# Kernel tuning notes

Measured on AMD Instinct MI355X. Metric: run time of the kernel, lower is better.

## Reference

```python
import jax, jax.numpy as jnp
import numpy as np

B, C, H, W = 4, 256, 64, 64
C8 = C // 8


def setup_inputs() -> dict:
    key = jax.random.key(0)
    k1, k2, k3, k4 = jax.random.split(key, 4)
    x = jax.random.normal(k1, (B, C, H, W), dtype=jnp.float32)
    # conv1d(ks=1, bias=False) projections -> plain [out, in] matrices
    Wq = jax.random.normal(k2, (C8, C), dtype=jnp.float32) * (1.0 / np.sqrt(C))
    Wk = jax.random.normal(k3, (C8, C), dtype=jnp.float32) * (1.0 / np.sqrt(C))
    Wv = jax.random.normal(k4, (C, C), dtype=jnp.float32) * (1.0 / np.sqrt(C))
    gamma = jnp.zeros((1,), dtype=jnp.float32)
    return {"x": x, "Wq": Wq, "Wk": Wk, "Wv": Wv, "gamma": gamma}


def reference(x, Wq, Wk, Wv, gamma):
    b, c, h, w = x.shape
    xf = x.reshape(b, c, h * w)                      # [B, C, N]
    f = jnp.einsum('oc,bcn->bon', Wq, xf)            # [B, C/8, N] query
    g = jnp.einsum('oc,bcn->bon', Wk, xf)            # [B, C/8, N] key
    hv = jnp.einsum('oc,bcn->bon', Wv, xf)           # [B, C,   N] value
    # scores[b,i,j] = sum_c f[b,c,i] * g[b,c,j]; softmax over dim=1 (i)
    scores = jnp.einsum('bci,bcj->bij', f, g)        # [B, N, N]
    beta = jax.nn.softmax(scores, axis=1)
    # o[b,c,j] = sum_i hv[b,c,i] * beta[b,i,j]
    o = jnp.einsum('bci,bij->bcj', hv, beta)         # [B, C, N]
    out = gamma[0] * o + xf
    return out.reshape(b, c, h, w)
```

## Files before the change

### kernel.cpp

```cpp
#include <hip/hip_runtime.h>

#define B_  4
#define C_  256
#define C8_ 32
#define N_  4096

#define TJ 128
#define KI 64
#define SPLITS 4

typedef __attribute__((ext_vector_type(8)))  short bf16x8;
typedef __attribute__((ext_vector_type(16))) float f32x16;

union FragAB { bf16x8 v; unsigned short u[8]; };

__device__ __forceinline__ unsigned short f2bf(float x) {
    unsigned u = __float_as_uint(x);
    unsigned r = u + 0x7FFFu + ((u >> 16) & 1u);
    return (unsigned short)(r >> 16);
}
__device__ __forceinline__ unsigned pack2bf(float a, float b) {
    return (unsigned)f2bf(a) | ((unsigned)f2bf(b) << 16);
}

__global__ __launch_bounds__(256) void prep_w_kernel(
    const float* __restrict__ Wq, const float* __restrict__ Wk,
    const float* __restrict__ Wv, unsigned short* __restrict__ Wbf)
{
    int idx = (blockIdx.x * 256 + threadIdx.x) * 4;
    int row = idx >> 8;
    int col = idx & 255;
    const float* src; int r;
    if (row < 32)      { src = Wq; r = row;      }
    else if (row < 64) { src = Wk; r = row - 32; }
    else               { src = Wv; r = row - 64; }
    float4 v = *(const float4*)&src[r * 256 + col];
    uint2 o; o.x = pack2bf(v.x, v.y); o.y = pack2bf(v.z, v.w);
    *(uint2*)&Wbf[idx] = o;
}

__global__ __launch_bounds__(256) void prep_x_kernel(
    const float* __restrict__ x, unsigned short* __restrict__ xT)
{
    __shared__ unsigned short T[64][66];
    int t  = threadIdx.x;
    int b  = blockIdx.z;
    int c0 = blockIdx.y * 64;
    int n0 = blockIdx.x * 64;
    const float* xb = x + (size_t)b * C_ * N_;
    int n_l = t & 63, c_l = t >> 6;
#pragma unroll
    for (int q = 0; q < 16; ++q) {
        int c = c_l * 16 + q;
        T[n_l][c] = f2bf(xb[(size_t)(c0 + c) * N_ + n0 + n_l]);
    }
    __syncthreads();
    unsigned short* xTb = xT + (size_t)b * N_ * C_;
    int c_l2 = t & 63, nb = t >> 6;
#pragma unroll
    for (int q = 0; q < 16; ++q) {
        int n = nb * 16 + q;
        xTb[(size_t)(n0 + n) * C_ + c0 + c_l2] = T[n][c_l2];
    }
}

__global__ __launch_bounds__(256) void proj_mfma_kernel(
    const unsigned short* __restrict__ Wbf, const unsigned short* __restrict__ xT,
    unsigned short* __restrict__ f, unsigned short* __restrict__ g,
    unsigned short* __restrict__ hv)
{
    int t = threadIdx.x, w = t >> 6, lane = t & 63;
    int half = lane >> 5, l31 = lane & 31;
    int b  = blockIdx.y;
    int n0 = blockIdx.x * 32;

    const unsigned short* xb = xT + ((size_t)b * N_ + n0 + l31) * C_;
    int nm = (w < 2) ? 3 : 2;
    int mt0 = w, mt1 = w + 4, mt2 = w + 8;

    f32x16 acc[3];
#pragma unroll
    for (int a = 0; a < 3; ++a) acc[a] = (f32x16)0.f;

#pragma unroll
    for (int ks = 0; ks < 16; ++ks) {
        int kofs = ks * 16 + half * 8;
        bf16x8 bfr = *(const bf16x8*)&xb[kofs];
        bf16x8 a0 = *(const bf16x8*)&Wbf[(size_t)(mt0 * 32 + l31) * 256 + kofs];
        acc[0] = __builtin_amdgcn_mfma_f32_32x32x16_bf16(a0, bfr, acc[0], 0, 0, 0);
        bf16x8 a1 = *(const bf16x8*)&Wbf[(size_t)(mt1 * 32 + l31) * 256 + kofs];
        acc[1] = __builtin_amdgcn_mfma_f32_32x32x16_bf16(a1, bfr, acc[1], 0, 0, 0);
        if (nm == 3) {
            bf16x8 a2 = *(const bf16x8*)&Wbf[(size_t)(mt2 * 32 + l31) * 256 + kofs];
            acc[2] = __builtin_amdgcn_mfma_f32_32x32x16_bf16(a2, bfr, acc[2], 0, 0, 0);
        }
    }

    unsigned short* fb = f  + (size_t)b * C8_ * N_;
    unsigned short* gb = g  + (size_t)b * C8_ * N_;
    unsigned short* hb = hv + (size_t)b * C_  * N_;
#pragma unroll
    for (int im = 0; im < 3; ++im) {
        if (im >= nm) break;
        int mt = (im == 0) ? mt0 : (im == 1) ? mt1 : mt2;
#pragma unroll
        for (int r = 0; r < 16; ++r) {
            int R = mt * 32 + (r & 3) + 8 * (r >> 2) + 4 * half;
            unsigned short v = f2bf(acc[im][r]);
            if (R < 32)       fb[(size_t)R * N_ + n0 + l31] = v;
            else if (R < 64)  gb[(size_t)(R - 64 + 32) * N_ + n0 + l31] = v;
            else              hb[(size_t)(R - 64) * N_ + n0 + l31] = v;
        }
    }
}

__global__ __launch_bounds__(256, 2) void flash_kernel(
    const unsigned short* __restrict__ f, const unsigned short* __restrict__ g,
    const unsigned short* __restrict__ hv, float* __restrict__ o_part,
    float* __restrict__ l_part)
{
    __shared__ unsigned short fT[64][40];
    __shared__ unsigned short hvT[256][72];
    __shared__ unsigned short pT[128][72];

    int t    = threadIdx.x;
    int w    = t >> 6;
    int lane = t & 63;
    int half = lane >> 5;
    int l31  = lane & 31;

    int b  = blockIdx.z;
    int s  = blockIdx.y;
    int j0 = blockIdx.x * TJ;

    const unsigned short* fb = f  + (size_t)b * C8_ * N_;
    const unsigned short* gb = g  + (size_t)b * C8_ * N_;
    const unsigned short* hb = hv + (size_t)b * C_  * N_;

    FragAB gf[2];
#pragma unroll
    for (int ks = 0; ks < 2; ++ks)
#pragma unroll
        for (int r = 0; r < 8; ++r) {
            int ch = ks * 16 + half * 8 + r;
            gf[ks].u[r] = gb[(size_t)ch * N_ + j0 + w * 32 + l31];
        }

    f32x16 acc[8];
#pragma unroll
    for (int a = 0; a < 8; ++a) acc[a] = (f32x16)0.f;
    float lacc = 0.f;

    int i_begin = s * (N_ / SPLITS);
    int i_end   = i_begin + N_ / SPLITS;

    for (int i0 = i_begin; i0 < i_end; i0 += KI) {
        __syncthreads();

        {
            int i   = t & 63;
            int chb = (t >> 6) * 8;
            unsigned short v[8];
#pragma unroll
            for (int q = 0; q < 8; ++q)
                v[q] = fb[(size_t)(chb + q) * N_ + i0 + i];
#pragma unroll
            for (int q = 0; q < 4; ++q)
                *(unsigned*)&fT[i][chb + 2 * q] =
                    (unsigned)v[2 * q] | ((unsigned)v[2 * q + 1] << 16);
        }
        {
            int crow  = t >> 3;
            int chunk = t & 7;
#pragma unroll
            for (int q = 0; q < 8; ++q) {
                int c = crow + 32 * q;
                uint4 v = *(const uint4*)&hb[(size_t)c * N_ + i0 + chunk * 8];
                *(uint4*)&hvT[c][chunk * 8] = v;
            }
        }
        __syncthreads();

#pragma unroll
        for (int it = 0; it < 2; ++it) {
            f32x16 sacc = (f32x16)0.f;
#pragma unroll
            for (int ks = 0; ks < 2; ++ks) {
                bf16x8 af = *(const bf16x8*)&fT[it * 32 + l31][ks * 16 + half * 8];
                sacc = __builtin_amdgcn_mfma_f32_32x32x16_bf16(af, gf[ks].v, sacc, 0, 0, 0);
            }
            float p[16];
#pragma unroll
            for (int r = 0; r < 16; ++r) {
                p[r] = __expf(sacc[r]);
                lacc += p[r];
            }
            int jr = w * 32 + l31;
#pragma unroll
            for (int a = 0; a < 4; ++a) {
                unsigned u0 = pack2bf(p[4 * a + 0], p[4 * a + 1]);
                unsigned u1 = pack2bf(p[4 * a + 2], p[4 * a + 3]);
                uint2 v; v.x = u0; v.y = u1;
                *(uint2*)&pT[jr][it * 32 + 8 * a + 4 * half] = v;
            }
        }
        __syncthreads();

#pragma unroll
        for (int ks4 = 0; ks4 < 4; ++ks4) {
            int kofs = ks4 * 16 + half * 8;
            bf16x8 af[2], bfr[4];
#pragma unroll
            for (int ct = 0; ct < 2; ++ct)
                af[ct] = *(const bf16x8*)&hvT[w * 64 + ct * 32 + l31][kofs];
#pragma unroll
            for (int jt = 0; jt < 4; ++jt)
                bfr[jt] = *(const bf16x8*)&pT[jt * 32 + l31][kofs];
#pragma unroll
            for (int ct = 0; ct < 2; ++ct)
#pragma unroll
                for (int jt = 0; jt < 4; ++jt)
                    acc[ct * 4 + jt] = __builtin_amdgcn_mfma_f32_32x32x16_bf16(
                        af[ct], bfr[jt], acc[ct * 4 + jt], 0, 0, 0);
        }
    }

    float* ob = o_part + (size_t)(b * SPLITS + s) * C_ * N_;
#pragma unroll
    for (int ct = 0; ct < 2; ++ct)
#pragma unroll
        for (int jt = 0; jt < 4; ++jt) {
            f32x16 a = acc[ct * 4 + jt];
#pragma unroll
            for (int r = 0; r < 16; ++r) {
                int c = w * 64 + ct * 32 + (r & 3) + 8 * (r >> 2) + 4 * half;
                int j = j0 + jt * 32 + l31;
                ob[(size_t)c * N_ + j] = a[r];
            }
        }
    float lsum = lacc + __shfl_down(lacc, 32);
    if (lane < 32)
        l_part[(size_t)(b * SPLITS + s) * N_ + j0 + w * 32 + lane] = lsum;
}

__global__ __launch_bounds__(256) void combine_kernel(
    const float* __restrict__ o_part, const float* __restrict__ l_part,
    const float* __restrict__ x, const float* __restrict__ gamma,
    float* __restrict__ out)
{
    int j = blockIdx.x * 256 + threadIdx.x;
    int b = blockIdx.z;
    float l = 0.f;
#pragma unroll
    for (int s = 0; s < SPLITS; ++s)
        l += l_part[(size_t)(b * SPLITS + s) * N_ + j];
    float inv = 1.f / l;
    float gm = gamma[0];
#pragma unroll
    for (int cc = 0; cc < 4; ++cc) {
        int c = blockIdx.y * 4 + cc;
        float o = 0.f;
#pragma unroll
        for (int s = 0; s < SPLITS; ++s)
            o += o_part[((size_t)(b * SPLITS + s) * C_ + c) * N_ + j];
        size_t idx = ((size_t)b * C_ + c) * N_ + j;
        out[idx] = gm * o * inv + x[idx];
    }
}

extern "C" void kernel_launch(void* const* d_in, const int* in_sizes, int n_in,
                              void* d_out, int out_size, void* d_ws, size_t ws_size,
                              hipStream_t stream) {
    const float* x     = (const float*)d_in[0];
    const float* Wq    = (const float*)d_in[1];
    const float* Wk    = (const float*)d_in[2];
    const float* Wv    = (const float*)d_in[3];
    const float* gamma = (const float*)d_in[4];
    float* out = (float*)d_out;

    char* ws = (char*)d_ws;
    float* o_part = (float*)ws;
    float* l_part = o_part + (size_t)SPLITS * B_ * C_ * N_;
    unsigned short* f   = (unsigned short*)(l_part + (size_t)SPLITS * B_ * N_);
    unsigned short* g   = f   + (size_t)B_ * C8_ * N_;
    unsigned short* hv  = g   + (size_t)B_ * C8_ * N_;
    unsigned short* Wbf = hv  + (size_t)B_ * C_  * N_;
    unsigned short* xT  = Wbf + (size_t)(C_ + 2 * C8_) * C_;

    prep_w_kernel<<<dim3(80), 256, 0, stream>>>(Wq, Wk, Wv, Wbf);
    prep_x_kernel<<<dim3(N_ / 64, C_ / 64, B_), 256, 0, stream>>>(x, xT);

    proj_mfma_kernel<<<dim3(N_ / 32, B_), 256, 0, stream>>>(Wbf, xT, f, g, hv);

    flash_kernel<<<dim3(N_ / TJ, SPLITS, B_), 256, 0, stream>>>(f, g, hv, o_part, l_part);

    combine_kernel<<<dim3(N_ / 256, C_ / 4, B_), 256, 0, stream>>>(o_part, l_part, x, gamma, out);
}
```

Measured before the change: 159.7 us.

## Restructure flash kernel: direct global hv/fT loads, bf16 partials, swizzled P, XCD block mapping

The projection now writes f transposed and hv with a padded row stride, so the flash kernel reads MFMA fragments straight from global memory instead of staging f and hv through LDS. Only the P tile stays in LDS, with an XOR swizzle and KI raised to 128, and one barrier pair per iteration. Partial outputs are stored as bf16 using the hardware pack instruction, halving partial-output traffic, and combine is vectorised to float4. The flash grid is remapped to a 1D index that groups blocks by batch and split, apparently aiming to improve L2 locality across XCDs. Risks are extra bf16 rounding in the partial sums and uncoalesced direct global fragment loads.

```diff
diff --git a/kernel.cpp b/kernel.cpp
--- a/kernel.cpp
+++ b/kernel.cpp
@@ -4,9 +4,10 @@
 #define C_  256
 #define C8_ 32
 #define N_  4096
+#define HVS_ (N_ + 64)
 
 #define TJ 128
-#define KI 64
+#define KI 128
 #define SPLITS 4
 
 typedef __attribute__((ext_vector_type(8)))  short bf16x8;
@@ -21,6 +22,11 @@
 }
 __device__ __forceinline__ unsigned pack2bf(float a, float b) {
     return (unsigned)f2bf(a) | ((unsigned)f2bf(b) << 16);
+}
+__device__ __forceinline__ unsigned cvtpk(float lo, float hi) {
+    unsigned r;
+    asm("v_cvt_pk_bf16_f32 %0, %1, %2" : "=v"(r) : "v"(lo), "v"(hi));
+    return r;
 }
 
 __global__ __launch_bounds__(256) void prep_w_kernel(
@@ -66,7 +72,7 @@
 
 __global__ __launch_bounds__(256) void proj_mfma_kernel(
     const unsigned short* __restrict__ Wbf, const unsigned short* __restrict__ xT,
-    unsigned short* __restrict__ f, unsigned short* __restrict__ g,
+    unsigned short* __restrict__ fT, unsigned short* __restrict__ g,
     unsigned short* __restrict__ hv)
 {
     int t = threadIdx.x, w = t >> 6, lane = t & 63;
@@ -96,46 +102,53 @@
         }
     }
 
-    unsigned short* fb = f  + (size_t)b * C8_ * N_;
-    unsigned short* gb = g  + (size_t)b * C8_ * N_;
-    unsigned short* hb = hv + (size_t)b * C_  * N_;
+    unsigned short* fTb = fT + (size_t)b * N_ * C8_;
+    unsigned short* gb  = g  + (size_t)b * C8_ * N_;
+    unsigned short* hb  = hv + (size_t)b * C_  * HVS_;
 #pragma unroll
     for (int im = 0; im < 3; ++im) {
         if (im >= nm) break;
         int mt = (im == 0) ? mt0 : (im == 1) ? mt1 : mt2;
-#pragma unroll
-        for (int r = 0; r < 16; ++r) {
-            int R = mt * 32 + (r & 3) + 8 * (r >> 2) + 4 * half;
-            unsigned short v = f2bf(acc[im][r]);
-            if (R < 32)       fb[(size_t)R * N_ + n0 + l31] = v;
-            else if (R < 64)  gb[(size_t)(R - 64 + 32) * N_ + n0 + l31] = v;
-            else              hb[(size_t)(R - 64) * N_ + n0 + l31] = v;
+        if (mt == 0) {
+#pragma unroll
+            for (int rp = 0; rp < 8; ++rp) {
+                int r = 2 * rp;
+                int R = (r & 3) + 8 * (r >> 2) + 4 * half;
+                unsigned u = pack2bf(acc[0][r], acc[0][r + 1]);
+                *(unsigned*)&fTb[(size_t)(n0 + l31) * C8_ + R] = u;
+            }
+        } else {
+#pragma unroll
+            for (int r = 0; r < 16; ++r) {
+                int R = mt * 32 + (r & 3) + 8 * (r >> 2) + 4 * half;
+                unsigned short v = f2bf(acc[im][r]);
+                if (R < 64) gb[(size_t)(R - 32) * N_ + n0 + l31] = v;
+                else        hb[(size_t)(R - 64) * HVS_ + n0 + l31] = v;
+            }
         }
     }
 }
 
 __global__ __launch_bounds__(256, 2) void flash_kernel(
-    const unsigned short* __restrict__ f, const unsigned short* __restrict__ g,
-    const unsigned short* __restrict__ hv, float* __restrict__ o_part,
+    const unsigned short* __restrict__ fT, const unsigned short* __restrict__ g,
+    const unsigned short* __restrict__ hv, unsigned short* __restrict__ o_part,
     float* __restrict__ l_part)
 {
-    __shared__ unsigned short fT[64][40];
-    __shared__ unsigned short hvT[256][72];
-    __shared__ unsigned short pT[128][72];
-
-    int t    = threadIdx.x;
-    int w    = t >> 6;
-    int lane = t & 63;
-    int half = lane >> 5;
-    int l31  = lane & 31;
-
-    int b  = blockIdx.z;
-    int s  = blockIdx.y;
-    int j0 = blockIdx.x * TJ;
-
-    const unsigned short* fb = f  + (size_t)b * C8_ * N_;
+    __shared__ unsigned short pT[TJ * KI];
+
+    int t = threadIdx.x, w = t >> 6, lane = t & 63;
+    int half = lane >> 5, l31 = lane & 31;
+
+    int d  = blockIdx.x;
+    int jb = (d >> 3) & 31;
+    int p  = (d & 7) | (((d >> 8) & 1) << 3);
+    int b  = p & 3;
+    int s  = p >> 2;
+    int j0 = jb * TJ;
+
+    const unsigned short* fb = fT + (size_t)b * N_ * C8_;
     const unsigned short* gb = g  + (size_t)b * C8_ * N_;
-    const unsigned short* hb = hv + (size_t)b * C_  * N_;
+    const unsigned short* hb = hv + (size_t)b * C_  * HVS_;
 
     FragAB gf[2];
 #pragma unroll
@@ -151,91 +164,77 @@
     for (int a = 0; a < 8; ++a) acc[a] = (f32x16)0.f;
     float lacc = 0.f;
 
+    const int swz = (l31 & 15) << 4;
+    const unsigned pbase = (unsigned)(w * 32 + l31) * (KI * 2);
+    char* pTc = (char*)pT;
+
+    const unsigned short* h0 = hb + (size_t)(w * 64 + l31) * HVS_ + half * 8;
+    const unsigned short* h1 = h0 + (size_t)32 * HVS_;
+
     int i_begin = s * (N_ / SPLITS);
-    int i_end   = i_begin + N_ / SPLITS;
-
-    for (int i0 = i_begin; i0 < i_end; i0 += KI) {
+
+    for (int ii = 0; ii < N_ / SPLITS; ii += KI) {
+        int i0 = i_begin + ii;
+
+#pragma unroll
+        for (int it = 0; it < 4; ++it) {
+            const unsigned short* fr = fb + (size_t)(i0 + it * 32 + l31) * C8_ + half * 8;
+            bf16x8 a0 = *(const bf16x8*)fr;
+            bf16x8 a1 = *(const bf16x8*)(fr + 16);
+            f32x16 sacc = (f32x16)0.f;
+            sacc = __builtin_amdgcn_mfma_f32_32x32x16_bf16(a0, gf[0].v, sacc, 0, 0, 0);
+            sacc = __builtin_amdgcn_mfma_f32_32x32x16_bf16(a1, gf[1].v, sacc, 0, 0, 0);
+            float pv[16];
+#pragma unroll
+            for (int r = 0; r < 16; ++r) {
+                pv[r] = __expf(sacc[r]);
+                lacc += pv[r];
+            }
+#pragma unroll
+            for (int a = 0; a < 4; ++a) {
+                uint2 u;
+                u.x = cvtpk(pv[4 * a + 0], pv[4 * a + 1]);
+                u.y = cvtpk(pv[4 * a + 2], pv[4 * a + 3]);
+                int ib = ((it * 64 + a * 16) ^ swz) + half * 8;
+                *(uint2*)(pTc + pbase + ib) = u;
+            }
+        }
         __syncthreads();
 
-        {
-            int i   = t & 63;
-            int chb = (t >> 6) * 8;
-            unsigned short v[8];
-#pragma unroll
-            for (int q = 0; q < 8; ++q)
-                v[q] = fb[(size_t)(chb + q) * N_ + i0 + i];
-#pragma unroll
-            for (int q = 0; q < 4; ++q)
-                *(unsigned*)&fT[i][chb + 2 * q] =
-                    (unsigned)v[2 * q] | ((unsigned)v[2 * q + 1] << 16);
-        }
-        {
-            int crow  = t >> 3;
-            int chunk = t & 7;
-#pragma unroll
-            for (int q = 0; q < 8; ++q) {
-                int c = crow + 32 * q;
-                uint4 v = *(const uint4*)&hb[(size_t)c * N_ + i0 + chunk * 8];
-                *(uint4*)&hvT[c][chunk * 8] = v;
+        const unsigned short* hp0 = h0 + i0;
+        const unsigned short* hp1 = h1 + i0;
+#pragma unroll
+        for (int ks = 0; ks < 8; ++ks) {
+            bf16x8 ah0 = *(const bf16x8*)(hp0 + ks * 16);
+            bf16x8 ah1 = *(const bf16x8*)(hp1 + ks * 16);
+            int ib = (ks * 32 + half * 16) ^ swz;
+            bf16x8 bp[4];
+#pragma unroll
+            for (int jt = 0; jt < 4; ++jt)
+                bp[jt] = *(const bf16x8*)(pTc + (jt * 32 + l31) * (KI * 2) + ib);
+#pragma unroll
+            for (int jt = 0; jt < 4; ++jt) {
+                acc[jt]     = __builtin_amdgcn_mfma_f32_32x32x16_bf16(ah0, bp[jt], acc[jt], 0, 0, 0);
+                acc[4 + jt] = __builtin_amdgcn_mfma_f32_32x32x16_bf16(ah1, bp[jt], acc[4 + jt], 0, 0, 0);
             }
         }
         __syncthreads();
-
-#pragma unroll
-        for (int it = 0; it < 2; ++it) {
-            f32x16 sacc = (f32x16)0.f;
-#pragma unroll
-            for (int ks = 0; ks < 2; ++ks) {
-                bf16x8 af = *(const bf16x8*)&fT[it * 32 + l31][ks * 16 + half * 8];
-                sacc = __builtin_amdgcn_mfma_f32_32x32x16_bf16(af, gf[ks].v, sacc, 0, 0, 0);
-            }
-            float p[16];
-#pragma unroll
-            for (int r = 0; r < 16; ++r) {
-                p[r] = __expf(sacc[r]);
-                lacc += p[r];
-            }
-            int jr = w * 32 + l31;
-#pragma unroll
-            for (int a = 0; a < 4; ++a) {
-                unsigned u0 = pack2bf(p[4 * a + 0], p[4 * a + 1]);
-                unsigned u1 = pack2bf(p[4 * a + 2], p[4 * a + 3]);
-                uint2 v; v.x = u0; v.y = u1;
-                *(uint2*)&pT[jr][it * 32 + 8 * a + 4 * half] = v;
-            }
-        }
-        __syncthreads();
-
-#pragma unroll
-        for (int ks4 = 0; ks4 < 4; ++ks4) {
-            int kofs = ks4 * 16 + half * 8;
-            bf16x8 af[2], bfr[4];
-#pragma unroll
-            for (int ct = 0; ct < 2; ++ct)
-                af[ct] = *(const bf16x8*)&hvT[w * 64 + ct * 32 + l31][kofs];
-#pragma unroll
-            for (int jt = 0; jt < 4; ++jt)
-                bfr[jt] = *(const bf16x8*)&pT[jt * 32 + l31][kofs];
-#pragma unroll
-            for (int ct = 0; ct < 2; ++ct)
-#pragma unroll
-                for (int jt = 0; jt < 4; ++jt)
-                    acc[ct * 4 + jt] = __builtin_amdgcn_mfma_f32_32x32x16_bf16(
-                        af[ct], bfr[jt], acc[ct * 4 + jt], 0, 0, 0);
-        }
-    }
-
-    float* ob = o_part + (size_t)(b * SPLITS + s) * C_ * N_;
+    }
+
+    unsigned short* ob = o_part + (size_t)(b * SPLITS + s) * C_ * N_;
 #pragma unroll
     for (int ct = 0; ct < 2; ++ct)
 #pragma unroll
         for (int jt = 0; jt < 4; ++jt) {
             f32x16 a = acc[ct * 4 + jt];
 #pragma unroll
-            for (int r = 0; r < 16; ++r) {
+            for (int rp = 0; rp < 8; ++rp) {
+                int r = 2 * rp;
+                unsigned u = cvtpk(a[r], a[r + 1]);
                 int c = w * 64 + ct * 32 + (r & 3) + 8 * (r >> 2) + 4 * half;
-                int j = j0 + jt * 32 + l31;
-                ob[(size_t)c * N_ + j] = a[r];
+                size_t base = (size_t)c * N_ + j0 + jt * 32 + l31;
+                ob[base]      = (unsigned short)(u & 0xffffu);
+                ob[base + N_] = (unsigned short)(u >> 16);
             }
         }
     float lsum = lacc + __shfl_down(lacc, 32);
@@ -244,27 +243,37 @@
 }
 
 __global__ __launch_bounds__(256) void combine_kernel(
-    const float* __restrict__ o_part, const float* __restrict__ l_part,
+    const unsigned short* __restrict__ o_part, const float* __restrict__ l_part,
     const float* __restrict__ x, const float* __restrict__ gamma,
     float* __restrict__ out)
 {
-    int j = blockIdx.x * 256 + threadIdx.x;
+    int j = (blockIdx.x * 256 + threadIdx.x) * 4;
     int b = blockIdx.z;
-    float l = 0.f;
-#pragma unroll
-    for (int s = 0; s < SPLITS; ++s)
-        l += l_part[(size_t)(b * SPLITS + s) * N_ + j];
-    float inv = 1.f / l;
+    float4 l4 = {0.f, 0.f, 0.f, 0.f};
+#pragma unroll
+    for (int s = 0; s < SPLITS; ++s) {
+        float4 lv = *(const float4*)&l_part[(size_t)(b * SPLITS + s) * N_ + j];
+        l4.x += lv.x; l4.y += lv.y; l4.z += lv.z; l4.w += lv.w;
+    }
+    float4 inv = {1.f / l4.x, 1.f / l4.y, 1.f / l4.z, 1.f / l4.w};
     float gm = gamma[0];
 #pragma unroll
     for (int cc = 0; cc < 4; ++cc) {
         int c = blockIdx.y * 4 + cc;
-        float o = 0.f;
-#pragma unroll
-        for (int s = 0; s < SPLITS; ++s)
-            o += o_part[((size_t)(b * SPLITS + s) * C_ + c) * N_ + j];
+        float4 o = {0.f, 0.f, 0.f, 0.f};
+#pragma unroll
+        for (int s = 0; s < SPLITS; ++s) {
+            uint2 u = *(const uint2*)&o_part[((size_t)(b * SPLITS + s) * C_ + c) * N_ + j];
+            o.x += __uint_as_float(u.x << 16);
+            o.y += __uint_as_float(u.x & 0xffff0000u);
+            o.z += __uint_as_float(u.y << 16);
+            o.w += __uint_as_float(u.y & 0xffff0000u);
+        }
         size_t idx = ((size_t)b * C_ + c) * N_ + j;
-        out[idx] = gm * o * inv + x[idx];
+        float4 xv = *(const float4*)&x[idx];
+        float4 st = {gm * o.x * inv.x + xv.x, gm * o.y * inv.y + xv.y,
+                     gm * o.z * inv.z + xv.z, gm * o.w * inv.w + xv.w};
+        *(float4*)&out[idx] = st;
     }
 }
 
@@ -279,20 +288,20 @@
     float* out = (float*)d_out;
 
     char* ws = (char*)d_ws;
-    float* o_part = (float*)ws;
-    float* l_part = o_part + (size_t)SPLITS * B_ * C_ * N_;
-    unsigned short* f   = (unsigned short*)(l_part + (size_t)SPLITS * B_ * N_);
-    unsigned short* g   = f   + (size_t)B_ * C8_ * N_;
+    unsigned short* o_part = (unsigned short*)ws;
+    float* l_part = (float*)(o_part + (size_t)SPLITS * B_ * C_ * N_);
+    unsigned short* fT  = (unsigned short*)(l_part + (size_t)SPLITS * B_ * N_);
+    unsigned short* g   = fT  + (size_t)B_ * C8_ * N_;
     unsigned short* hv  = g   + (size_t)B_ * C8_ * N_;
-    unsigned short* Wbf = hv  + (size_t)B_ * C_  * N_;
+    unsigned short* Wbf = hv  + (size_t)B_ * C_  * HVS_;
     unsigned short* xT  = Wbf + (size_t)(C_ + 2 * C8_) * C_;
 
     prep_w_kernel<<<dim3(80), 256, 0, stream>>>(Wq, Wk, Wv, Wbf);
     prep_x_kernel<<<dim3(N_ / 64, C_ / 64, B_), 256, 0, stream>>>(x, xT);
 
-    proj_mfma_kernel<<<dim3(N_ / 32, B_), 256, 0, stream>>>(Wbf, xT, f, g, hv);
-
-    flash_kernel<<<dim3(N_ / TJ, SPLITS, B_), 256, 0, stream>>>(f, g, hv, o_part, l_part);
-
-    combine_kernel<<<dim3(N_ / 256, C_ / 4, B_), 256, 0, stream>>>(o_part, l_part, x, gamma, out);
-}
+    proj_mfma_kernel<<<dim3(N_ / 32, B_), 256, 0, stream>>>(Wbf, xT, fT, g, hv);
+
+    flash_kernel<<<dim3(512), 256, 0, stream>>>(fT, g, hv, o_part, l_part);
+
+    combine_kernel<<<dim3(N_ / 1024, C_ / 4, B_), 256, 0, stream>>>(o_part, l_part, x, gamma, out);
+}
```

After: 160.0 us. No clear change (+0.2%).
